# Performance work log

Hardware: AMD Instinct MI355X
Metric: run time of the kernel (lower is better)

Reference implementation:

```python
import jax, jax.numpy as jnp
import numpy as np

B, S, H = 2, 2048, 1024
NH, HD = 16, 64  # n_heads, head_dim


def setup_inputs() -> dict:
    key = jax.random.key(0)
    ks = jax.random.split(key, 9)
    d = {}
    d['query'] = jax.random.normal(ks[0], (B, S, H), dtype=jnp.float32)
    d['key'] = jax.random.normal(ks[1], (B, S, H), dtype=jnp.float32)
    d['value'] = jax.random.normal(ks[2], (B, S, H), dtype=jnp.float32)
    s = 1.0 / np.sqrt(H)
    d['Wq'] = jax.random.normal(ks[3], (H, H), dtype=jnp.float32) * s
    d['bq'] = jax.random.normal(ks[4], (H,), dtype=jnp.float32) * s
    d['Wk'] = jax.random.normal(ks[5], (H, H), dtype=jnp.float32) * s
    d['bk'] = jax.random.normal(ks[6], (H,), dtype=jnp.float32) * s
    d['Wv'] = jax.random.normal(ks[7], (H, H), dtype=jnp.float32) * s
    d['bv'] = jax.random.normal(ks[8], (H,), dtype=jnp.float32) * s
    return d


def reference(query, key, value, Wq, bq, Wk, bk, Wv, bv):
    b, s, h = query.shape
    # torch Linear: y = x @ W.T + b
    Q = query @ Wq.T + bq
    K = key @ Wk.T + bk
    V = value @ Wv.T + bv
    # Faithful to the source: reshape [B,S,H] -> [B,NH,S,HD] directly (no
    # transpose), i.e. 'heads' are contiguous sequence chunks, as in the
    # original module's reshape(batch_size, n_heads, -1, head_dim).
    Q = Q.reshape(b, NH, s, HD)
    K = K.reshape(b, NH, s, HD)
    V = V.reshape(b, NH, s, HD)
    scale = jnp.sqrt(jnp.asarray(HD, dtype=Q.dtype))
    energy = jnp.einsum('bnqd,bnkd->bnqk', Q, K) / scale  # [B,NH,S,S]
    attention = jax.nn.softmax(energy, axis=-1)
    x = jnp.einsum('bnqk,bnkd->bnqd', attention, V)  # [B,NH,S,HD]
    x = x.transpose(0, 2, 1, 3).reshape(b, s, h)
    # Source computes `x - fc_o(x)` but discards the result; output is x.
    return x
```

## Files before the change

kernel.cpp:

```cpp
#include <hip/hip_runtime.h>


typedef short s16x8 __attribute__((ext_vector_type(8)));
typedef float f32x4 __attribute__((ext_vector_type(4)));
typedef float f32x16 __attribute__((ext_vector_type(16)));
typedef unsigned int u32x2 __attribute__((ext_vector_type(2)));
typedef unsigned int u32x4 __attribute__((ext_vector_type(4)));
typedef float f32x4u __attribute__((ext_vector_type(4), aligned(4)));

#define MFMA16(a, b, c) __builtin_amdgcn_mfma_f32_16x16x32_bf16((a), (b), (c), 0, 0, 0)
#define MFMA32(a, b, c) __builtin_amdgcn_mfma_f32_32x32x16_bf16((a), (b), (c), 0, 0, 0)

__device__ __forceinline__ short f2bf(float f) {
  unsigned u = __builtin_bit_cast(unsigned, f);
  u = (u + 0x7fffu + ((u >> 16) & 1u)) >> 16;
  return (short)u;
}

__device__ __forceinline__ float exp2v(float x) {
  float r;
  asm("v_exp_f32 %0, %1" : "=v"(r) : "v"(x));
  return r;
}

#define QSCALE (0.125f * 1.44269504088896340736f)

struct CvtArgs {
  const float* X[3];
  const float* W[3];
  short* Xb;
  short* Wb;
};

__global__ __launch_bounds__(256) void cvt_kernel(CvtArgs a) {
  const size_t t = (size_t)blockIdx.x * 256 + threadIdx.x;
  const size_t e = t * 8;
  const float* src;
  short* dst;
  size_t off;
  if (e < (size_t)3 * 4194304) {
    src = a.X[e >> 22];
    off = e & 4194303;
    dst = a.Xb + e;
  } else {
    const size_t e2 = e - (size_t)3 * 4194304;
    src = a.W[e2 >> 20];
    off = e2 & 1048575;
    dst = a.Wb + e2;
  }
  f32x4 v0 = *(const f32x4*)(src + off);
  f32x4 v1 = *(const f32x4*)(src + off + 4);
  s16x8 o;
#pragma unroll
  for (int j = 0; j < 4; ++j) { o[j] = f2bf(v0[j]); o[j + 4] = f2bf(v1[j]); }
  *(s16x8*)dst = o;
}

struct Gemm2Args {
  const short* Xb;
  const short* Wb;
  const float* Bv[3];
  short* Y[3];
  float scale[3];
};

__global__ __launch_bounds__(256) void qkv_gemm_bf16(Gemm2Args a) {
  const int L = (blockIdx.x & 7) * 96 + (blockIdx.x >> 3);
  const int n_t = L & 7;
  const int m_t = (L >> 3) & 31;
  const int z = L >> 8;

  const short* __restrict__ Xz = a.Xb + (size_t)z * 4096 * 1024;
  const short* __restrict__ Wz = a.Wb + (size_t)z * 1024 * 1024;
  const float* __restrict__ Bv = a.Bv[z];
  short* __restrict__ Y = a.Y[z];
  const float scale = a.scale[z];

  __shared__ __align__(16) short Smem[2][2][8192];

  const int tid = threadIdx.x;
  const int lane = tid & 63;
  const int wave = tid >> 6;
  const int m0 = m_t * 128;
  const int n0 = n_t * 128;
  const int moff = (wave >> 1) * 64;
  const int noff = (wave & 1) * 64;
  const int fr = lane & 15;
  const int fk = (lane >> 4) * 8;

  const int srow = lane >> 3;
  const int scol = (lane & 7) * 8;

  f32x4 acc[4][4] = {};

  auto stage = [&](int buf, int k0) {
#pragma unroll
    for (int i = 0; i < 4; ++i) {
      const int c = wave * 4 + i;
      const short* ga = Xz + (size_t)(m0 + c * 8 + srow) * 1024 + k0 + scol;
      const short* gb = Wz + (size_t)(n0 + c * 8 + srow) * 1024 + k0 + scol;
      __builtin_amdgcn_global_load_lds(
          (const __attribute__((address_space(1))) unsigned int*)ga,
          (__attribute__((address_space(3))) unsigned int*)&Smem[buf][0][c * 512], 16, 0, 0);
      __builtin_amdgcn_global_load_lds(
          (const __attribute__((address_space(1))) unsigned int*)gb,
          (__attribute__((address_space(3))) unsigned int*)&Smem[buf][1][c * 512], 16, 0, 0);
    }
  };

  stage(0, 0);
  for (int t = 0; t < 16; ++t) {
    const int buf = t & 1;
    if (t < 15) {
      stage(buf ^ 1, (t + 1) * 64);
      asm volatile("s_waitcnt vmcnt(8)" ::: "memory");
    } else {
      asm volatile("s_waitcnt vmcnt(0)" ::: "memory");
    }
    __builtin_amdgcn_s_barrier();
    __builtin_amdgcn_sched_barrier(0);

    const short* Asb = &Smem[buf][0][0];
    const short* Bsb = &Smem[buf][1][0];
#pragma unroll
    for (int kk = 0; kk < 64; kk += 32) {
      s16x8 af[4], bf[4];
#pragma unroll
      for (int i = 0; i < 4; ++i) af[i] = *(const s16x8*)&Asb[(moff + i * 16 + fr) * 64 + kk + fk];
#pragma unroll
      for (int j = 0; j < 4; ++j) bf[j] = *(const s16x8*)&Bsb[(noff + j * 16 + fr) * 64 + kk + fk];
#pragma unroll
      for (int i = 0; i < 4; ++i)
#pragma unroll
        for (int j = 0; j < 4; ++j)
          acc[i][j] = MFMA16(af[i], bf[j], acc[i][j]);
    }
    __builtin_amdgcn_s_barrier();
    __builtin_amdgcn_sched_barrier(0);
  }

  short* Cs = &Smem[0][0][0];
  const int l16 = lane >> 4;
#pragma unroll
  for (int j = 0; j < 4; ++j) {
    const int col = noff + j * 16 + fr;
    const float bias = Bv[n0 + col];
#pragma unroll
    for (int i = 0; i < 4; ++i) {
      const int rowb = moff + i * 16 + l16 * 4;
#pragma unroll
      for (int r = 0; r < 4; ++r)
        Cs[(rowb + r) * 136 + col] = f2bf((acc[i][j][r] + bias) * scale);
    }
  }
  __syncthreads();
  {
    const int row = tid >> 1;
    const int c0 = (tid & 1) * 64;
    short* dst = Y + (size_t)(m0 + row) * 1024 + n0 + c0;
    const short* src = &Cs[row * 136 + c0];
#pragma unroll
    for (int p = 0; p < 8; ++p)
      *(s16x8*)(dst + p * 8) = *(const s16x8*)(src + p * 8);
  }
}

struct ProjArgs {
  const float* X[3];
  const float* W[3];
  const float* Bv[3];
  short* Y[3];
  float scale[3];
};

#define PBM 128
#define PBN 128
#define PBK 32
#define PLD (PBK + 8)

__global__ __launch_bounds__(256) void qkv_proj_fallback(ProjArgs args) {
  const int z = blockIdx.z;
  const float* __restrict__ X = args.X[z];
  const float* __restrict__ W = args.W[z];
  const float* __restrict__ Bv = args.Bv[z];
  short* __restrict__ Y = args.Y[z];
  const float scale = args.scale[z];

  __shared__ __align__(16) short As[PBM][PLD];
  __shared__ __align__(16) short Bs[PBN][PLD];

  const int tid = threadIdx.x;
  const int lane = tid & 63;
  const int wave = tid >> 6;
  const int m0 = blockIdx.y * PBM;
  const int n0 = blockIdx.x * PBN;
  const int moff = (wave >> 1) * 64;
  const int noff = (wave & 1) * 64;
  const int fr = lane & 15;
  const int fk = (lane >> 4) * 8;

  const int srow = tid >> 1;
  const int scol = (tid & 1) * 16;

  f32x4 acc[4][4] = {};

  const float* ap = X + (size_t)(m0 + srow) * 1024 + scol;
  const float* bp = W + (size_t)(n0 + srow) * 1024 + scol;

  for (int k0 = 0; k0 < 1024; k0 += PBK) {
    f32x4 a0 = *(const f32x4*)(ap + k0);
    f32x4 a1 = *(const f32x4*)(ap + k0 + 4);
    f32x4 a2 = *(const f32x4*)(ap + k0 + 8);
    f32x4 a3 = *(const f32x4*)(ap + k0 + 12);
    f32x4 b0 = *(const f32x4*)(bp + k0);
    f32x4 b1 = *(const f32x4*)(bp + k0 + 4);
    f32x4 b2 = *(const f32x4*)(bp + k0 + 8);
    f32x4 b3 = *(const f32x4*)(bp + k0 + 12);

    s16x8 sa0, sa1, sb0, sb1;
#pragma unroll
    for (int j = 0; j < 4; ++j) {
      sa0[j] = f2bf(a0[j]); sa0[j + 4] = f2bf(a1[j]);
      sa1[j] = f2bf(a2[j]); sa1[j + 4] = f2bf(a3[j]);
      sb0[j] = f2bf(b0[j]); sb0[j + 4] = f2bf(b1[j]);
      sb1[j] = f2bf(b2[j]); sb1[j + 4] = f2bf(b3[j]);
    }

    __syncthreads();
    *(s16x8*)&As[srow][scol]     = sa0;
    *(s16x8*)&As[srow][scol + 8] = sa1;
    *(s16x8*)&Bs[srow][scol]     = sb0;
    *(s16x8*)&Bs[srow][scol + 8] = sb1;
    __syncthreads();

    s16x8 af[4], bfm[4];
#pragma unroll
    for (int i = 0; i < 4; ++i) af[i] = *(const s16x8*)&As[moff + i * 16 + fr][fk];
#pragma unroll
    for (int j = 0; j < 4; ++j) bfm[j] = *(const s16x8*)&Bs[noff + j * 16 + fr][fk];
#pragma unroll
    for (int i = 0; i < 4; ++i)
#pragma unroll
      for (int j = 0; j < 4; ++j)
        acc[i][j] = MFMA16(af[i], bfm[j], acc[i][j]);
  }

#pragma unroll
  for (int j = 0; j < 4; ++j) {
    const int col = n0 + noff + j * 16 + fr;
    const float bias = Bv[col];
#pragma unroll
    for (int i = 0; i < 4; ++i) {
      const int rowb = m0 + moff + i * 16 + (lane >> 4) * 4;
#pragma unroll
      for (int r = 0; r < 4; ++r) {
        Y[(size_t)(rowb + r) * 1024 + col] = f2bf((acc[i][j][r] + bias) * scale);
      }
    }
  }
}

#define TRR(dst, base, OFF) \
  asm volatile("ds_read_b64_tr_b16 %0, %1 offset:" OFF : "=v"(dst) : "v"(base))

__global__ __launch_bounds__(256, 2) void attn_kernel(
    const short* __restrict__ Qb, const short* __restrict__ Kb,
    const short* __restrict__ Vb, float* __restrict__ out) {
  const int head = blockIdx.x;
  const int bz = blockIdx.y;
  const int qb = blockIdx.z;

  const size_t hb = (size_t)bz * (2048 * 1024) + (size_t)head * (2048 * 64);
  const short* __restrict__ Qh = Qb + hb;
  const short* __restrict__ Kh = Kb + hb;
  const short* __restrict__ Vh = Vb + hb;

  __shared__ __align__(16) short Klds[2][4096];
  __shared__ __align__(16) short Vlds[2][4096];

  const int tid = threadIdx.x;
  const int lane = tid & 63;
  const int wave = tid >> 6;
  const int l31 = lane & 31;
  const int hi = lane >> 5;

  const int q0w = qb * 128 + wave * 32;
  s16x8 qf[4];
#pragma unroll
  for (int f = 0; f < 4; ++f)
    qf[f] = *(const s16x8*)(Qh + (size_t)(q0w + l31) * 64 + f * 16 + hi * 8);

  const int kr = tid >> 2;
  const int kc = (tid & 3) * 16;
  const int ksw = (kr & 7) << 4;
  const int kb0 = kr * 128 + ((kc * 2) ^ ksw);
  const int kb1 = kr * 128 + ((kc * 2 + 16) ^ ksw);
  const int vd0 = (tid & 3) * 16 + (((tid >> 4) & 1) * 8);
  const int vd1 = vd0 ^ 8;
  const int vb0w = ((kr >> 2) * 4 + (vd0 >> 4)) * 128 + (kr & 3) * 32 + (vd0 & 15) * 2;
  const int vb1w = ((kr >> 2) * 4 + (vd1 >> 4)) * 128 + (kr & 3) * 32 + (vd1 & 15) * 2;

  int cXor[4];
#pragma unroll
  for (int f = 0; f < 4; ++f) cXor[f] = ((f * 32 + hi * 16) ^ ((l31 & 7) << 4));

  const unsigned vlane = (unsigned)(hi * 1024 + ((l31 >> 4) * 128) + (lane & 15) * 8);

  s16x8 kn0 = *(const s16x8*)(Kh + kr * 64 + kc);
  s16x8 kn1 = *(const s16x8*)(Kh + kr * 64 + kc + 8);
  s16x8 vn0 = *(const s16x8*)(Vh + kr * 64 + vd0);
  s16x8 vn1 = *(const s16x8*)(Vh + kr * 64 + vd1);
  *(s16x8*)((char*)&Klds[0][0] + kb0) = kn0;
  *(s16x8*)((char*)&Klds[0][0] + kb1) = kn1;
  *(s16x8*)((char*)&Vlds[0][0] + vb0w) = vn0;
  *(s16x8*)((char*)&Vlds[0][0] + vb1w) = vn1;

  float m = -1e30f, lsum = 0.f;
  f32x16 acc0 = {}, acc1 = {};

  for (int t = 0; t < 32; ++t) {
    __syncthreads();
    const int cur = t & 1;

    if (t < 31) {
      const short* kg = Kh + (size_t)(t + 1) * 4096 + kr * 64 + kc;
      kn0 = *(const s16x8*)kg;
      kn1 = *(const s16x8*)(kg + 8);
      const short* vg = Vh + (size_t)(t + 1) * 4096 + kr * 64;
      vn0 = *(const s16x8*)(vg + vd0);
      vn1 = *(const s16x8*)(vg + vd1);
    }

    const char* kl = (const char*)&Klds[cur][0];
    f32x16 et0 = {}, et1 = {};
    __builtin_amdgcn_s_setprio(1);
#pragma unroll
    for (int f = 0; f < 4; ++f) {
      s16x8 kf = *(const s16x8*)(kl + l31 * 128 + cXor[f]);
      et0 = MFMA32(kf, qf[f], et0);
    }
#pragma unroll
    for (int f = 0; f < 4; ++f) {
      s16x8 kf = *(const s16x8*)(kl + 4096 + l31 * 128 + cXor[f]);
      et1 = MFMA32(kf, qf[f], et1);
    }
    __builtin_amdgcn_s_setprio(0);

    float mx[16];
#pragma unroll
    for (int r = 0; r < 16; ++r) mx[r] = fmaxf(et0[r], et1[r]);
#pragma unroll
    for (int s2 = 8; s2 >= 1; s2 >>= 1)
#pragma unroll
      for (int r = 0; r < 8; ++r)
        if (r < s2) mx[r] = fmaxf(mx[r], mx[r + s2]);
    if (__any(mx[0] > m + 8.f)) {
      const float mt = fmaxf(mx[0], __shfl_xor(mx[0], 32));
      const float mnew = fmaxf(m, mt);
      const float corr = exp2v(m - mnew);
      lsum *= corr;
      acc0 *= corr;
      acc1 *= corr;
      m = mnew;
    }

    float p0a[16], p1a[16], sm[16];
#pragma unroll
    for (int r = 0; r < 16; ++r) {
      p0a[r] = exp2v(et0[r] - m);
      p1a[r] = exp2v(et1[r] - m);
      sm[r] = p0a[r] + p1a[r];
    }
#pragma unroll
    for (int s2 = 8; s2 >= 1; s2 >>= 1)
#pragma unroll
      for (int r = 0; r < 8; ++r)
        if (r < s2) sm[r] += sm[r + s2];
    lsum += sm[0] + __shfl_xor(sm[0], 32);

    unsigned xr[2][4], yr[2][4];
#pragma unroll
    for (int c = 0; c < 4; ++c) {
      asm("v_cvt_pk_bf16_f32 %0, %1, %2" : "=v"(xr[0][c]) : "v"(p0a[4 * c + 0]), "v"(p0a[4 * c + 1]));
      asm("v_cvt_pk_bf16_f32 %0, %1, %2" : "=v"(yr[0][c]) : "v"(p0a[4 * c + 2]), "v"(p0a[4 * c + 3]));
      asm("v_cvt_pk_bf16_f32 %0, %1, %2" : "=v"(xr[1][c]) : "v"(p1a[4 * c + 0]), "v"(p1a[4 * c + 1]));
      asm("v_cvt_pk_bf16_f32 %0, %1, %2" : "=v"(yr[1][c]) : "v"(p1a[4 * c + 2]), "v"(p1a[4 * c + 3]));
    }
    s16x8 pf[4];
#pragma unroll
    for (int T = 0; T < 2; ++T)
#pragma unroll
      for (int u = 0; u < 2; ++u) {
        unsigned w0 = xr[T][2 * u], w2 = xr[T][2 * u + 1];
        unsigned w1 = yr[T][2 * u], w3 = yr[T][2 * u + 1];
        asm("v_permlane32_swap_b32 %0, %1" : "+v"(w0), "+v"(w2));
        asm("v_permlane32_swap_b32 %0, %1" : "+v"(w1), "+v"(w3));
        u32x4 w = {w0, w1, w2, w3};
        pf[2 * T + u] = __builtin_bit_cast(s16x8, w);
      }

    const unsigned vb = (unsigned)(size_t)((const char*)&Vlds[cur][0]) + vlane;
    u32x2 va[2][4][2];
    TRR(va[0][0][0], vb, "0");    TRR(va[0][0][1], vb, "512");
    TRR(va[0][1][0], vb, "2048"); TRR(va[0][1][1], vb, "2560");
    TRR(va[0][2][0], vb, "4096"); TRR(va[0][2][1], vb, "4608");
    TRR(va[0][3][0], vb, "6144"); TRR(va[0][3][1], vb, "6656");
    TRR(va[1][0][0], vb, "256");  TRR(va[1][0][1], vb, "768");
    TRR(va[1][1][0], vb, "2304"); TRR(va[1][1][1], vb, "2816");
    TRR(va[1][2][0], vb, "4352"); TRR(va[1][2][1], vb, "4864");
    TRR(va[1][3][0], vb, "6400"); TRR(va[1][3][1], vb, "6912");
    asm volatile("s_waitcnt lgkmcnt(0)" ::: "memory");
    __builtin_amdgcn_sched_barrier(0);
    __builtin_amdgcn_s_setprio(1);
#pragma unroll
    for (int k0i = 0; k0i < 4; ++k0i) {
      u32x4 w0 = {va[0][k0i][0][0], va[0][k0i][0][1], va[0][k0i][1][0], va[0][k0i][1][1]};
      u32x4 w1 = {va[1][k0i][0][0], va[1][k0i][0][1], va[1][k0i][1][0], va[1][k0i][1][1]};
      acc0 = MFMA32(__builtin_bit_cast(s16x8, w0), pf[k0i], acc0);
      acc1 = MFMA32(__builtin_bit_cast(s16x8, w1), pf[k0i], acc1);
    }
    __builtin_amdgcn_s_setprio(0);

    if (t < 31) {
      char* kld = (char*)&Klds[cur ^ 1][0];
      char* vld = (char*)&Vlds[cur ^ 1][0];
      *(s16x8*)(kld + kb0) = kn0;
      *(s16x8*)(kld + kb1) = kn1;
      *(s16x8*)(vld + vb0w) = vn0;
      *(s16x8*)(vld + vb1w) = vn1;
    }
  }

  const float inv = 1.0f / lsum;
  acc0 *= inv;
  acc1 *= inv;
  float* op = out + ((size_t)bz * 2048 + q0w + l31) * 1024 + head * 64;
#pragma unroll
  for (int c = 0; c < 4; ++c) {
    f32x4u v0 = {acc0[4 * c + 0], acc0[4 * c + 1], acc0[4 * c + 2], acc0[4 * c + 3]};
    f32x4u v1 = {acc1[4 * c + 0], acc1[4 * c + 1], acc1[4 * c + 2], acc1[4 * c + 3]};
    *(f32x4u*)(op + 8 * c + 4 * hi) = v0;
    *(f32x4u*)(op + 32 + 8 * c + 4 * hi) = v1;
  }
}

extern "C" void kernel_launch(void* const* d_in, const int* in_sizes, int n_in,
                              void* d_out, int out_size, void* d_ws, size_t ws_size,
                              hipStream_t stream) {
  const float* query = (const float*)d_in[0];
  const float* key   = (const float*)d_in[1];
  const float* value = (const float*)d_in[2];
  const float* Wq = (const float*)d_in[3];
  const float* bq = (const float*)d_in[4];
  const float* Wk = (const float*)d_in[5];
  const float* bk = (const float*)d_in[6];
  const float* Wv = (const float*)d_in[7];
  const float* bv = (const float*)d_in[8];
  float* out = (float*)d_out;

  short* Qw = (short*)d_ws;
  short* Kw = Qw + (size_t)4096 * 1024;
  short* Vw = Kw + (size_t)4096 * 1024;
  short* Xb = Vw + (size_t)4096 * 1024;
  short* Wb = Xb + (size_t)3 * 4096 * 1024;

  const size_t need = ((size_t)6 * 4096 * 1024 + (size_t)3 * 1024 * 1024) * 2;

  if (ws_size >= need) {
    CvtArgs ca;
    ca.X[0] = query; ca.X[1] = key; ca.X[2] = value;
    ca.W[0] = Wq; ca.W[1] = Wk; ca.W[2] = Wv;
    ca.Xb = Xb; ca.Wb = Wb;
    cvt_kernel<<<7680, 256, 0, stream>>>(ca);

    Gemm2Args ga;
    ga.Xb = Xb; ga.Wb = Wb;
    ga.Bv[0] = bq; ga.Bv[1] = bk; ga.Bv[2] = bv;
    ga.Y[0] = Qw; ga.Y[1] = Kw; ga.Y[2] = Vw;
    ga.scale[0] = QSCALE; ga.scale[1] = 1.0f; ga.scale[2] = 1.0f;
    qkv_gemm_bf16<<<768, 256, 0, stream>>>(ga);
  } else {
    ProjArgs pa;
    pa.X[0] = query; pa.X[1] = key; pa.X[2] = value;
    pa.W[0] = Wq; pa.W[1] = Wk; pa.W[2] = Wv;
    pa.Bv[0] = bq; pa.Bv[1] = bk; pa.Bv[2] = bv;
    pa.Y[0] = Qw; pa.Y[1] = Kw; pa.Y[2] = Vw;
    pa.scale[0] = QSCALE; pa.scale[1] = 1.0f; pa.scale[2] = 1.0f;
    qkv_proj_fallback<<<dim3(1024 / PBN, 4096 / PBM, 3), 256, 0, stream>>>(pa);
  }

  attn_kernel<<<dim3(16, 2, 16), 256, 0, stream>>>(Qw, Kw, Vw, out);
}
```

Before: 116.2 us.

## Split attention KV range across two wave groups and swizzle GEMM LDS tiles

The attention kernel now runs 512 threads per block. Two groups of four waves each process half of the key/value sequence, with separate double-buffered LDS tiles. Their partial softmax states are merged through LDS at the end, which doubles the waves available per query tile and should improve latency hiding. Separately, the QKV GEMM applies an XOR swizzle to LDS column placement and to the matching fragment reads, to reduce bank conflicts. The changes add an extra reduction phase, more LDS, and tighter register limits from launch_bounds(512,4).

```diff
diff --git a/kernel.cpp b/kernel.cpp
--- a/kernel.cpp
+++ b/kernel.cpp
@@ -87,9 +87,10 @@
   const int noff = (wave & 1) * 64;
   const int fr = lane & 15;
   const int fk = (lane >> 4) * 8;
+  const int fsw = (fr & 7) * 8;
 
   const int srow = lane >> 3;
-  const int scol = (lane & 7) * 8;
+  const int scolX = ((lane & 7) ^ (lane >> 3)) * 8;
 
   f32x4 acc[4][4] = {};
 
@@ -97,8 +98,8 @@
 #pragma unroll
     for (int i = 0; i < 4; ++i) {
       const int c = wave * 4 + i;
-      const short* ga = Xz + (size_t)(m0 + c * 8 + srow) * 1024 + k0 + scol;
-      const short* gb = Wz + (size_t)(n0 + c * 8 + srow) * 1024 + k0 + scol;
+      const short* ga = Xz + (size_t)(m0 + c * 8 + srow) * 1024 + k0 + scolX;
+      const short* gb = Wz + (size_t)(n0 + c * 8 + srow) * 1024 + k0 + scolX;
       __builtin_amdgcn_global_load_lds(
           (const __attribute__((address_space(1))) unsigned int*)ga,
           (__attribute__((address_space(3))) unsigned int*)&Smem[buf][0][c * 512], 16, 0, 0);
@@ -126,9 +127,11 @@
     for (int kk = 0; kk < 64; kk += 32) {
       s16x8 af[4], bf[4];
 #pragma unroll
-      for (int i = 0; i < 4; ++i) af[i] = *(const s16x8*)&Asb[(moff + i * 16 + fr) * 64 + kk + fk];
-#pragma unroll
-      for (int j = 0; j < 4; ++j) bf[j] = *(const s16x8*)&Bsb[(noff + j * 16 + fr) * 64 + kk + fk];
+      for (int i = 0; i < 4; ++i)
+        af[i] = *(const s16x8*)&Asb[(moff + i * 16 + fr) * 64 + ((kk + fk) ^ fsw)];
+#pragma unroll
+      for (int j = 0; j < 4; ++j)
+        bf[j] = *(const s16x8*)&Bsb[(noff + j * 16 + fr) * 64 + ((kk + fk) ^ fsw)];
 #pragma unroll
       for (int i = 0; i < 4; ++i)
 #pragma unroll
@@ -263,7 +266,7 @@
 #define TRR(dst, base, OFF) \
   asm volatile("ds_read_b64_tr_b16 %0, %1 offset:" OFF : "=v"(dst) : "v"(base))
 
-__global__ __launch_bounds__(256, 2) void attn_kernel(
+__global__ __launch_bounds__(512, 4) void attn_kernel(
     const short* __restrict__ Qb, const short* __restrict__ Kb,
     const short* __restrict__ Vb, float* __restrict__ out) {
   const int head = blockIdx.x;
@@ -275,27 +278,29 @@
   const short* __restrict__ Kh = Kb + hb;
   const short* __restrict__ Vh = Vb + hb;
 
-  __shared__ __align__(16) short Klds[2][4096];
-  __shared__ __align__(16) short Vlds[2][4096];
+  __shared__ __align__(16) short Klds[2][2][4096];
+  __shared__ __align__(16) short Vlds[2][2][4096];
 
   const int tid = threadIdx.x;
   const int lane = tid & 63;
-  const int wave = tid >> 6;
+  const int g = tid >> 8;
+  const int gtid = tid & 255;
+  const int w4 = (tid >> 6) & 3;
   const int l31 = lane & 31;
   const int hi = lane >> 5;
 
-  const int q0w = qb * 128 + wave * 32;
+  const int q0w = qb * 128 + w4 * 32;
   s16x8 qf[4];
 #pragma unroll
   for (int f = 0; f < 4; ++f)
     qf[f] = *(const s16x8*)(Qh + (size_t)(q0w + l31) * 64 + f * 16 + hi * 8);
 
-  const int kr = tid >> 2;
-  const int kc = (tid & 3) * 16;
+  const int kr = gtid >> 2;
+  const int kc = (gtid & 3) * 16;
   const int ksw = (kr & 7) << 4;
   const int kb0 = kr * 128 + ((kc * 2) ^ ksw);
   const int kb1 = kr * 128 + ((kc * 2 + 16) ^ ksw);
-  const int vd0 = (tid & 3) * 16 + (((tid >> 4) & 1) * 8);
+  const int vd0 = (gtid & 3) * 16 + (((gtid >> 4) & 1) * 8);
   const int vd1 = vd0 ^ 8;
   const int vb0w = ((kr >> 2) * 4 + (vd0 >> 4)) * 128 + (kr & 3) * 32 + (vd0 & 15) * 2;
   const int vb1w = ((kr >> 2) * 4 + (vd1 >> 4)) * 128 + (kr & 3) * 32 + (vd1 & 15) * 2;
@@ -306,32 +311,34 @@
 
   const unsigned vlane = (unsigned)(hi * 1024 + ((l31 >> 4) * 128) + (lane & 15) * 8);
 
-  s16x8 kn0 = *(const s16x8*)(Kh + kr * 64 + kc);
-  s16x8 kn1 = *(const s16x8*)(Kh + kr * 64 + kc + 8);
-  s16x8 vn0 = *(const s16x8*)(Vh + kr * 64 + vd0);
-  s16x8 vn1 = *(const s16x8*)(Vh + kr * 64 + vd1);
-  *(s16x8*)((char*)&Klds[0][0] + kb0) = kn0;
-  *(s16x8*)((char*)&Klds[0][0] + kb1) = kn1;
-  *(s16x8*)((char*)&Vlds[0][0] + vb0w) = vn0;
-  *(s16x8*)((char*)&Vlds[0][0] + vb1w) = vn1;
+  const short* Kg0 = Kh + (size_t)(g * 16) * 4096;
+  const short* Vg0 = Vh + (size_t)(g * 16) * 4096;
+  s16x8 kn0 = *(const s16x8*)(Kg0 + kr * 64 + kc);
+  s16x8 kn1 = *(const s16x8*)(Kg0 + kr * 64 + kc + 8);
+  s16x8 vn0 = *(const s16x8*)(Vg0 + kr * 64 + vd0);
+  s16x8 vn1 = *(const s16x8*)(Vg0 + kr * 64 + vd1);
+  *(s16x8*)((char*)&Klds[g][0][0] + kb0) = kn0;
+  *(s16x8*)((char*)&Klds[g][0][0] + kb1) = kn1;
+  *(s16x8*)((char*)&Vlds[g][0][0] + vb0w) = vn0;
+  *(s16x8*)((char*)&Vlds[g][0][0] + vb1w) = vn1;
 
   float m = -1e30f, lsum = 0.f;
   f32x16 acc0 = {}, acc1 = {};
 
-  for (int t = 0; t < 32; ++t) {
+  for (int t = 0; t < 16; ++t) {
     __syncthreads();
     const int cur = t & 1;
 
-    if (t < 31) {
-      const short* kg = Kh + (size_t)(t + 1) * 4096 + kr * 64 + kc;
+    if (t < 15) {
+      const short* kg = Kh + (size_t)(g * 16 + t + 1) * 4096 + kr * 64 + kc;
       kn0 = *(const s16x8*)kg;
       kn1 = *(const s16x8*)(kg + 8);
-      const short* vg = Vh + (size_t)(t + 1) * 4096 + kr * 64;
+      const short* vg = Vh + (size_t)(g * 16 + t + 1) * 4096 + kr * 64;
       vn0 = *(const s16x8*)(vg + vd0);
       vn1 = *(const s16x8*)(vg + vd1);
     }
 
-    const char* kl = (const char*)&Klds[cur][0];
+    const char* kl = (const char*)&Klds[g][cur][0];
     f32x16 et0 = {}, et1 = {};
     __builtin_amdgcn_s_setprio(1);
 #pragma unroll
@@ -399,7 +406,7 @@
         pf[2 * T + u] = __builtin_bit_cast(s16x8, w);
       }
 
-    const unsigned vb = (unsigned)(size_t)((const char*)&Vlds[cur][0]) + vlane;
+    const unsigned vb = (unsigned)(size_t)((const char*)&Vlds[g][cur][0]) + vlane;
     u32x2 va[2][4][2];
     TRR(va[0][0][0], vb, "0");    TRR(va[0][0][1], vb, "512");
     TRR(va[0][1][0], vb, "2048"); TRR(va[0][1][1], vb, "2560");
@@ -421,9 +428,9 @@
     }
     __builtin_amdgcn_s_setprio(0);
 
-    if (t < 31) {
-      char* kld = (char*)&Klds[cur ^ 1][0];
-      char* vld = (char*)&Vlds[cur ^ 1][0];
+    if (t < 15) {
+      char* kld = (char*)&Klds[g][cur ^ 1][0];
+      char* vld = (char*)&Vlds[g][cur ^ 1][0];
       *(s16x8*)(kld + kb0) = kn0;
       *(s16x8*)(kld + kb1) = kn1;
       *(s16x8*)(vld + vb0w) = vn0;
@@ -431,16 +438,36 @@
     }
   }
 
-  const float inv = 1.0f / lsum;
-  acc0 *= inv;
-  acc1 *= inv;
-  float* op = out + ((size_t)bz * 2048 + q0w + l31) * 1024 + head * 64;
-#pragma unroll
-  for (int c = 0; c < 4; ++c) {
-    f32x4u v0 = {acc0[4 * c + 0], acc0[4 * c + 1], acc0[4 * c + 2], acc0[4 * c + 3]};
-    f32x4u v1 = {acc1[4 * c + 0], acc1[4 * c + 1], acc1[4 * c + 2], acc1[4 * c + 3]};
-    *(f32x4u*)(op + 8 * c + 4 * hi) = v0;
-    *(f32x4u*)(op + 32 + 8 * c + 4 * hi) = v1;
+  __syncthreads();
+  float* sc = (float*)&Klds[0][0][0];
+  float* ml = (float*)&Vlds[0][0][0];
+  if (g == 1) {
+#pragma unroll
+    for (int r = 0; r < 16; ++r) {
+      sc[r * 256 + gtid] = acc0[r];
+      sc[(16 + r) * 256 + gtid] = acc1[r];
+    }
+    ml[gtid] = m;
+    ml[256 + gtid] = lsum;
+  }
+  __syncthreads();
+  if (g == 0) {
+    const float m1 = ml[gtid], l1 = ml[256 + gtid];
+    const float mf = fmaxf(m, m1);
+    const float c0 = exp2v(m - mf), c1 = exp2v(m1 - mf);
+    const float linv = 1.0f / (lsum * c0 + l1 * c1);
+    float* op = out + ((size_t)bz * 2048 + q0w + l31) * 1024 + head * 64;
+#pragma unroll
+    for (int c = 0; c < 4; ++c) {
+      f32x4u v0, v1;
+#pragma unroll
+      for (int r2 = 0; r2 < 4; ++r2) {
+        v0[r2] = (acc0[4 * c + r2] * c0 + sc[(4 * c + r2) * 256 + gtid] * c1) * linv;
+        v1[r2] = (acc1[4 * c + r2] * c0 + sc[(16 + 4 * c + r2) * 256 + gtid] * c1) * linv;
+      }
+      *(f32x4u*)(op + 8 * c + 4 * hi) = v0;
+      *(f32x4u*)(op + 32 + 8 * c + 4 * hi) = v1;
+    }
   }
 }
 
@@ -489,5 +516,5 @@
     qkv_proj_fallback<<<dim3(1024 / PBN, 4096 / PBM, 3), 256, 0, stream>>>(pa);
   }
 
-  attn_kernel<<<dim3(16, 2, 16), 256, 0, stream>>>(Qw, Kw, Vw, out);
-}
+  attn_kernel<<<dim3(16, 2, 16), 512, 0, stream>>>(Qw, Kw, Vw, out);
+}
```

New measurement: 114.7 us. No clear change (-1.3%).

## Use async global-to-LDS loads with 128-key tiles and swizzled GEMM LDS layout

Applied to the files above, without the earlier changes.

The attention kernel now stages K and V tiles with global_load_lds straight into LDS instead of going through registers, and doubles the key tile from 64 to 128 rows, halving the number of loop iterations and barriers. The second half of the V transposed reads is issued during the first PV MFMAs, and max reductions use v_max3. The projection GEMM gets an XOR-swizzled LDS layout to cut bank conflicts. The trade is twice the LDS per block (possibly lowering occupancy), more live registers from four score tiles, and a missing explicit vmcnt wait before the barrier, which may make the async loads unsafe.

```diff
diff --git a/kernel.cpp b/kernel.cpp
--- a/kernel.cpp
+++ b/kernel.cpp
@@ -20,6 +20,12 @@
 __device__ __forceinline__ float exp2v(float x) {
   float r;
   asm("v_exp_f32 %0, %1" : "=v"(r) : "v"(x));
+  return r;
+}
+
+__device__ __forceinline__ float max3f(float a, float b, float c) {
+  float r;
+  asm("v_max3_f32 %0, %1, %2, %3" : "=v"(r) : "v"(a), "v"(b), "v"(c));
   return r;
 }
 
@@ -87,9 +93,10 @@
   const int noff = (wave & 1) * 64;
   const int fr = lane & 15;
   const int fk = (lane >> 4) * 8;
+  const int fsw = (fr & 7) * 8;
 
   const int srow = lane >> 3;
-  const int scol = (lane & 7) * 8;
+  const int scolX = ((lane & 7) ^ (lane >> 3)) * 8;
 
   f32x4 acc[4][4] = {};
 
@@ -97,8 +104,8 @@
 #pragma unroll
     for (int i = 0; i < 4; ++i) {
       const int c = wave * 4 + i;
-      const short* ga = Xz + (size_t)(m0 + c * 8 + srow) * 1024 + k0 + scol;
-      const short* gb = Wz + (size_t)(n0 + c * 8 + srow) * 1024 + k0 + scol;
+      const short* ga = Xz + (size_t)(m0 + c * 8 + srow) * 1024 + k0 + scolX;
+      const short* gb = Wz + (size_t)(n0 + c * 8 + srow) * 1024 + k0 + scolX;
       __builtin_amdgcn_global_load_lds(
           (const __attribute__((address_space(1))) unsigned int*)ga,
           (__attribute__((address_space(3))) unsigned int*)&Smem[buf][0][c * 512], 16, 0, 0);
@@ -126,9 +133,11 @@
     for (int kk = 0; kk < 64; kk += 32) {
       s16x8 af[4], bf[4];
 #pragma unroll
-      for (int i = 0; i < 4; ++i) af[i] = *(const s16x8*)&Asb[(moff + i * 16 + fr) * 64 + kk + fk];
-#pragma unroll
-      for (int j = 0; j < 4; ++j) bf[j] = *(const s16x8*)&Bsb[(noff + j * 16 + fr) * 64 + kk + fk];
+      for (int i = 0; i < 4; ++i)
+        af[i] = *(const s16x8*)&Asb[(moff + i * 16 + fr) * 64 + ((kk + fk) ^ fsw)];
+#pragma unroll
+      for (int j = 0; j < 4; ++j)
+        bf[j] = *(const s16x8*)&Bsb[(noff + j * 16 + fr) * 64 + ((kk + fk) ^ fsw)];
 #pragma unroll
       for (int i = 0; i < 4; ++i)
 #pragma unroll
@@ -275,8 +284,8 @@
   const short* __restrict__ Kh = Kb + hb;
   const short* __restrict__ Vh = Vb + hb;
 
-  __shared__ __align__(16) short Klds[2][4096];
-  __shared__ __align__(16) short Vlds[2][4096];
+  __shared__ __align__(16) short Klds[2][8192];
+  __shared__ __align__(16) short Vlds[2][8192];
 
   const int tid = threadIdx.x;
   const int lane = tid & 63;
@@ -290,15 +299,9 @@
   for (int f = 0; f < 4; ++f)
     qf[f] = *(const s16x8*)(Qh + (size_t)(q0w + l31) * 64 + f * 16 + hi * 8);
 
-  const int kr = tid >> 2;
-  const int kc = (tid & 3) * 16;
-  const int ksw = (kr & 7) << 4;
-  const int kb0 = kr * 128 + ((kc * 2) ^ ksw);
-  const int kb1 = kr * 128 + ((kc * 2 + 16) ^ ksw);
-  const int vd0 = (tid & 3) * 16 + (((tid >> 4) & 1) * 8);
-  const int vd1 = vd0 ^ 8;
-  const int vb0w = ((kr >> 2) * 4 + (vd0 >> 4)) * 128 + (kr & 3) * 32 + (vd0 & 15) * 2;
-  const int vb1w = ((kr >> 2) * 4 + (vd1 >> 4)) * 128 + (kr & 3) * 32 + (vd1 & 15) * 2;
+  const int ksrcl = (lane >> 3) * 64 + (((lane & 7) ^ (lane >> 3)) * 8);
+  const int vsrcl = ((lane >> 5) * 4 + ((lane & 7) >> 1)) * 64 +
+                    ((lane >> 3) & 3) * 16 + (lane & 1) * 8;
 
   int cXor[4];
 #pragma unroll
@@ -306,56 +309,68 @@
 
   const unsigned vlane = (unsigned)(hi * 1024 + ((l31 >> 4) * 128) + (lane & 15) * 8);
 
-  s16x8 kn0 = *(const s16x8*)(Kh + kr * 64 + kc);
-  s16x8 kn1 = *(const s16x8*)(Kh + kr * 64 + kc + 8);
-  s16x8 vn0 = *(const s16x8*)(Vh + kr * 64 + vd0);
-  s16x8 vn1 = *(const s16x8*)(Vh + kr * 64 + vd1);
-  *(s16x8*)((char*)&Klds[0][0] + kb0) = kn0;
-  *(s16x8*)((char*)&Klds[0][0] + kb1) = kn1;
-  *(s16x8*)((char*)&Vlds[0][0] + vb0w) = vn0;
-  *(s16x8*)((char*)&Vlds[0][0] + vb1w) = vn1;
+  auto stage = [&](int buf, int tile) {
+#pragma unroll
+    for (int i = 0; i < 4; ++i) {
+      const int c = wave * 4 + i;
+      const short* ks = Kh + (size_t)tile * 8192 + c * 512 + ksrcl;
+      const short* vs = Vh + (size_t)tile * 8192 + c * 512 + vsrcl;
+      __builtin_amdgcn_global_load_lds(
+          (const __attribute__((address_space(1))) unsigned int*)ks,
+          (__attribute__((address_space(3))) unsigned int*)&Klds[buf][c * 512], 16, 0, 0);
+      __builtin_amdgcn_global_load_lds(
+          (const __attribute__((address_space(1))) unsigned int*)vs,
+          (__attribute__((address_space(3))) unsigned int*)&Vlds[buf][c * 512], 16, 0, 0);
+    }
+  };
+
+  stage(0, 0);
 
   float m = -1e30f, lsum = 0.f;
   f32x16 acc0 = {}, acc1 = {};
 
-  for (int t = 0; t < 32; ++t) {
+  for (int t = 0; t < 16; ++t) {
     __syncthreads();
     const int cur = t & 1;
-
-    if (t < 31) {
-      const short* kg = Kh + (size_t)(t + 1) * 4096 + kr * 64 + kc;
-      kn0 = *(const s16x8*)kg;
-      kn1 = *(const s16x8*)(kg + 8);
-      const short* vg = Vh + (size_t)(t + 1) * 4096 + kr * 64;
-      vn0 = *(const s16x8*)(vg + vd0);
-      vn1 = *(const s16x8*)(vg + vd1);
-    }
+    if (t < 15) stage(cur ^ 1, t + 1);
 
     const char* kl = (const char*)&Klds[cur][0];
-    f32x16 et0 = {}, et1 = {};
+    f32x16 et[4] = {};
     __builtin_amdgcn_s_setprio(1);
 #pragma unroll
-    for (int f = 0; f < 4; ++f) {
-      s16x8 kf = *(const s16x8*)(kl + l31 * 128 + cXor[f]);
-      et0 = MFMA32(kf, qf[f], et0);
-    }
-#pragma unroll
-    for (int f = 0; f < 4; ++f) {
-      s16x8 kf = *(const s16x8*)(kl + 4096 + l31 * 128 + cXor[f]);
-      et1 = MFMA32(kf, qf[f], et1);
-    }
+    for (int X = 0; X < 4; ++X)
+#pragma unroll
+      for (int f = 0; f < 4; ++f) {
+        s16x8 kf = *(const s16x8*)(kl + X * 4096 + l31 * 128 + cXor[f]);
+        et[X] = MFMA32(kf, qf[f], et[X]);
+      }
     __builtin_amdgcn_s_setprio(0);
 
+    const unsigned vb = (unsigned)(size_t)((const char*)&Vlds[cur][0]) + vlane;
+    u32x2 vaA[2][4][2];
+    TRR(vaA[0][0][0], vb, "0");    TRR(vaA[0][0][1], vb, "512");
+    TRR(vaA[0][1][0], vb, "2048"); TRR(vaA[0][1][1], vb, "2560");
+    TRR(vaA[0][2][0], vb, "4096"); TRR(vaA[0][2][1], vb, "4608");
+    TRR(vaA[0][3][0], vb, "6144"); TRR(vaA[0][3][1], vb, "6656");
+    TRR(vaA[1][0][0], vb, "256");  TRR(vaA[1][0][1], vb, "768");
+    TRR(vaA[1][1][0], vb, "2304"); TRR(vaA[1][1][1], vb, "2816");
+    TRR(vaA[1][2][0], vb, "4352"); TRR(vaA[1][2][1], vb, "4864");
+    TRR(vaA[1][3][0], vb, "6400"); TRR(vaA[1][3][1], vb, "6912");
+
     float mx[16];
 #pragma unroll
-    for (int r = 0; r < 16; ++r) mx[r] = fmaxf(et0[r], et1[r]);
-#pragma unroll
-    for (int s2 = 8; s2 >= 1; s2 >>= 1)
-#pragma unroll
-      for (int r = 0; r < 8; ++r)
-        if (r < s2) mx[r] = fmaxf(mx[r], mx[r + s2]);
-    if (__any(mx[0] > m + 8.f)) {
-      const float mt = fmaxf(mx[0], __shfl_xor(mx[0], 32));
+    for (int r = 0; r < 16; ++r)
+      mx[r] = max3f(et[0][r], et[1][r], fmaxf(et[2][r], et[3][r]));
+    const float u0 = max3f(mx[0], mx[1], mx[2]);
+    const float u1 = max3f(mx[3], mx[4], mx[5]);
+    const float u2 = max3f(mx[6], mx[7], mx[8]);
+    const float u3 = max3f(mx[9], mx[10], mx[11]);
+    const float u4 = max3f(mx[12], mx[13], mx[14]);
+    const float u5 = max3f(u0, u1, mx[15]);
+    const float u6 = max3f(u2, u3, u4);
+    const float tmax = fmaxf(u5, u6);
+    if (__any(tmax > m + 8.f)) {
+      const float mt = fmaxf(tmax, __shfl_xor(tmax, 32));
       const float mnew = fmaxf(m, mt);
       const float corr = exp2v(m - mnew);
       lsum *= corr;
@@ -364,71 +379,72 @@
       m = mnew;
     }
 
-    float p0a[16], p1a[16], sm[16];
-#pragma unroll
-    for (int r = 0; r < 16; ++r) {
-      p0a[r] = exp2v(et0[r] - m);
-      p1a[r] = exp2v(et1[r] - m);
-      sm[r] = p0a[r] + p1a[r];
-    }
-#pragma unroll
-    for (int s2 = 8; s2 >= 1; s2 >>= 1)
-#pragma unroll
-      for (int r = 0; r < 8; ++r)
-        if (r < s2) sm[r] += sm[r + s2];
-    lsum += sm[0] + __shfl_xor(sm[0], 32);
-
-    unsigned xr[2][4], yr[2][4];
-#pragma unroll
-    for (int c = 0; c < 4; ++c) {
-      asm("v_cvt_pk_bf16_f32 %0, %1, %2" : "=v"(xr[0][c]) : "v"(p0a[4 * c + 0]), "v"(p0a[4 * c + 1]));
-      asm("v_cvt_pk_bf16_f32 %0, %1, %2" : "=v"(yr[0][c]) : "v"(p0a[4 * c + 2]), "v"(p0a[4 * c + 3]));
-      asm("v_cvt_pk_bf16_f32 %0, %1, %2" : "=v"(xr[1][c]) : "v"(p1a[4 * c + 0]), "v"(p1a[4 * c + 1]));
-      asm("v_cvt_pk_bf16_f32 %0, %1, %2" : "=v"(yr[1][c]) : "v"(p1a[4 * c + 2]), "v"(p1a[4 * c + 3]));
-    }
-    s16x8 pf[4];
-#pragma unroll
-    for (int T = 0; T < 2; ++T)
+    float sacc[16];
+    s16x8 pfA[4], pfB[4];
+#pragma unroll
+    for (int T = 0; T < 4; ++T) {
+      float pv[16];
+#pragma unroll
+      for (int r = 0; r < 16; ++r) {
+        pv[r] = exp2v(et[T][r] - m);
+        if (T == 0) sacc[r] = pv[r]; else sacc[r] += pv[r];
+      }
+      unsigned xr[4], yr[4];
+#pragma unroll
+      for (int c = 0; c < 4; ++c) {
+        asm("v_cvt_pk_bf16_f32 %0, %1, %2" : "=v"(xr[c]) : "v"(pv[4 * c + 0]), "v"(pv[4 * c + 1]));
+        asm("v_cvt_pk_bf16_f32 %0, %1, %2" : "=v"(yr[c]) : "v"(pv[4 * c + 2]), "v"(pv[4 * c + 3]));
+      }
 #pragma unroll
       for (int u = 0; u < 2; ++u) {
-        unsigned w0 = xr[T][2 * u], w2 = xr[T][2 * u + 1];
-        unsigned w1 = yr[T][2 * u], w3 = yr[T][2 * u + 1];
+        unsigned w0 = xr[2 * u], w2 = xr[2 * u + 1];
+        unsigned w1 = yr[2 * u], w3 = yr[2 * u + 1];
         asm("v_permlane32_swap_b32 %0, %1" : "+v"(w0), "+v"(w2));
         asm("v_permlane32_swap_b32 %0, %1" : "+v"(w1), "+v"(w3));
         u32x4 w = {w0, w1, w2, w3};
-        pf[2 * T + u] = __builtin_bit_cast(s16x8, w);
+        if (T < 2) pfA[2 * T + u] = __builtin_bit_cast(s16x8, w);
+        else       pfB[2 * (T - 2) + u] = __builtin_bit_cast(s16x8, w);
       }
-
-    const unsigned vb = (unsigned)(size_t)((const char*)&Vlds[cur][0]) + vlane;
-    u32x2 va[2][4][2];
-    TRR(va[0][0][0], vb, "0");    TRR(va[0][0][1], vb, "512");
-    TRR(va[0][1][0], vb, "2048"); TRR(va[0][1][1], vb, "2560");
-    TRR(va[0][2][0], vb, "4096"); TRR(va[0][2][1], vb, "4608");
-    TRR(va[0][3][0], vb, "6144"); TRR(va[0][3][1], vb, "6656");
-    TRR(va[1][0][0], vb, "256");  TRR(va[1][0][1], vb, "768");
-    TRR(va[1][1][0], vb, "2304"); TRR(va[1][1][1], vb, "2816");
-    TRR(va[1][2][0], vb, "4352"); TRR(va[1][2][1], vb, "4864");
-    TRR(va[1][3][0], vb, "6400"); TRR(va[1][3][1], vb, "6912");
+    }
+#pragma unroll
+    for (int s2 = 8; s2 >= 1; s2 >>= 1)
+#pragma unroll
+      for (int r = 0; r < 8; ++r)
+        if (r < s2) sacc[r] += sacc[r + s2];
+    lsum += sacc[0] + __shfl_xor(sacc[0], 32);
+
+    asm volatile("s_waitcnt lgkmcnt(0)" ::: "memory");
+    __builtin_amdgcn_sched_barrier(0);
+    u32x2 vaB[2][4][2];
+    TRR(vaB[0][0][0], vb, "8192");  TRR(vaB[0][0][1], vb, "8704");
+    TRR(vaB[0][1][0], vb, "10240"); TRR(vaB[0][1][1], vb, "10752");
+    TRR(vaB[0][2][0], vb, "12288"); TRR(vaB[0][2][1], vb, "12800");
+    TRR(vaB[0][3][0], vb, "14336"); TRR(vaB[0][3][1], vb, "14848");
+    TRR(vaB[1][0][0], vb, "8448");  TRR(vaB[1][0][1], vb, "8960");
+    TRR(vaB[1][1][0], vb, "10496"); TRR(vaB[1][1][1], vb, "11008");
+    TRR(vaB[1][2][0], vb, "12544"); TRR(vaB[1][2][1], vb, "13056");
+    TRR(vaB[1][3][0], vb, "14592"); TRR(vaB[1][3][1], vb, "15104");
+    __builtin_amdgcn_s_setprio(1);
+#pragma unroll
+    for (int k0i = 0; k0i < 4; ++k0i) {
+      u32x4 w0 = {vaA[0][k0i][0][0], vaA[0][k0i][0][1], vaA[0][k0i][1][0], vaA[0][k0i][1][1]};
+      u32x4 w1 = {vaA[1][k0i][0][0], vaA[1][k0i][0][1], vaA[1][k0i][1][0], vaA[1][k0i][1][1]};
+      acc0 = MFMA32(__builtin_bit_cast(s16x8, w0), pfA[k0i], acc0);
+      acc1 = MFMA32(__builtin_bit_cast(s16x8, w1), pfA[k0i], acc1);
+    }
+    __builtin_amdgcn_s_setprio(0);
+
     asm volatile("s_waitcnt lgkmcnt(0)" ::: "memory");
     __builtin_amdgcn_sched_barrier(0);
     __builtin_amdgcn_s_setprio(1);
 #pragma unroll
     for (int k0i = 0; k0i < 4; ++k0i) {
-      u32x4 w0 = {va[0][k0i][0][0], va[0][k0i][0][1], va[0][k0i][1][0], va[0][k0i][1][1]};
-      u32x4 w1 = {va[1][k0i][0][0], va[1][k0i][0][1], va[1][k0i][1][0], va[1][k0i][1][1]};
-      acc0 = MFMA32(__builtin_bit_cast(s16x8, w0), pf[k0i], acc0);
-      acc1 = MFMA32(__builtin_bit_cast(s16x8, w1), pf[k0i], acc1);
+      u32x4 w0 = {vaB[0][k0i][0][0], vaB[0][k0i][0][1], vaB[0][k0i][1][0], vaB[0][k0i][1][1]};
+      u32x4 w1 = {vaB[1][k0i][0][0], vaB[1][k0i][0][1], vaB[1][k0i][1][0], vaB[1][k0i][1][1]};
+      acc0 = MFMA32(__builtin_bit_cast(s16x8, w0), pfB[k0i], acc0);
+      acc1 = MFMA32(__builtin_bit_cast(s16x8, w1), pfB[k0i], acc1);
     }
     __builtin_amdgcn_s_setprio(0);
-
-    if (t < 31) {
-      char* kld = (char*)&Klds[cur ^ 1][0];
-      char* vld = (char*)&Vlds[cur ^ 1][0];
-      *(s16x8*)(kld + kb0) = kn0;
-      *(s16x8*)(kld + kb1) = kn1;
-      *(s16x8*)(vld + vb0w) = vn0;
-      *(s16x8*)(vld + vb1w) = vn1;
-    }
   }
 
   const float inv = 1.0f / lsum;
```

Result: faster. 104.9 us (-9.7%).
